# Performance work log

Hardware: AMD Instinct MI355X
Metric: run time of the kernel (lower is better)

The kernel has to match this reference:

```python
import jax, jax.numpy as jnp
import numpy as np

B, S, C, H = 2, 4096, 1024, 16
DH = C // H  # 64
# diffusers: attn.scale = dim_head ** -0.5; code divides scores by scale**0.5
SCALE = 1.0 / (float(DH) ** -0.25)  # == DH ** 0.25


def setup_inputs() -> dict:
    key = jax.random.key(0)
    ks = jax.random.split(key, 6)
    w = 0.02
    return {
        "hidden_states": jax.random.normal(ks[0], (B, S, C), jnp.float32),
        "Wq": jax.random.normal(ks[1], (C, C), jnp.float32) * w,
        "Wk": jax.random.normal(ks[2], (C, C), jnp.float32) * w,
        "Wv": jax.random.normal(ks[3], (C, C), jnp.float32) * w,
        "Wo": jax.random.normal(ks[4], (C, C), jnp.float32) * w,
        "bo": jnp.zeros((C,), jnp.float32),
        # token sizes >= 1 (number of patches each token represents)
        "token_sizes": jax.random.randint(ks[5], (B, S), 1, 17, jnp.int32),
    }


def _split_heads(x):
    # [B, S, C] -> [B, H, S, DH]
    return x.reshape(B, S, H, DH).transpose(0, 2, 1, 3)


def reference(hidden_states, Wq, Wk, Wv, Wo, bo, token_sizes):
    q = _split_heads(hidden_states @ Wq)  # [B,H,S,DH]
    k = _split_heads(hidden_states @ Wk)
    v = _split_heads(hidden_states @ Wv)
    # QK^T with diffusers-style scaling: scores / attn.scale**0.5 == scores * DH**0.25
    scores = jnp.einsum("bhqd,bhkd->bhqk", q, k) * SCALE  # [B,H,S,S]
    # additive log(token_size) bias over keys (self-attention path)
    log_sizes = jnp.log(token_sizes.astype(jnp.float32))  # [B,S]
    scores = scores + log_sizes[:, None, None, :]
    probs = jax.nn.softmax(scores, axis=-1)
    out = jnp.einsum("bhqk,bhkd->bhqd", probs, v)  # [B,H,S,DH]
    out = out.transpose(0, 2, 1, 3).reshape(B, S, C)  # merge heads
    return out @ Wo + bo  # to_out[0] linear; to_out[1] dropout is identity
```

## Files before the change

kernel.cpp:

```cpp
#include <hip/hip_runtime.h>


typedef unsigned short u16;
typedef unsigned int u32;
typedef _Float16 f16x8 __attribute__((ext_vector_type(8)));
typedef float f32x4 __attribute__((ext_vector_type(4)));
typedef short short4v __attribute__((ext_vector_type(4)));

constexpr int SEQ = 4096, CDIM = 1024, NH = 16, DHE = 64;
constexpr float SCALE2 = 2.8284271247461903f * 1.4426950408889634f;

union Frag { f16x8 v; short4v h[2]; };

__device__ __forceinline__ u16 f2h(float f) {
  union { _Float16 h; u16 u; } x;
  x.h = (_Float16)f;
  return x.u;
}

__device__ __forceinline__ u32 pkrtz(float a, float b) {
  u32 r;
  asm("v_cvt_pkrtz_f16_f32 %0, %1, %2" : "=v"(r) : "v"(a), "v"(b));
  return r;
}

__device__ __forceinline__ short4v pk4(const f32x4& v) {
  union { u32 w[2]; short4v s; } u;
  u.w[0] = pkrtz(v[0], v[1]);
  u.w[1] = pkrtz(v[2], v[3]);
  return u.s;
}

__device__ __forceinline__ float exp2fast(float x) {
  float r;
  asm("v_exp_f32 %0, %1" : "=v"(r) : "v"(x));
  return r;
}

__device__ __forceinline__ f32x4 mfma16(const Frag& a, const Frag& b, f32x4 c) {
  return __builtin_amdgcn_mfma_f32_16x16x32_f16(a.v, b.v, c, 0, 0, 0);
}


__global__ void cast_x_kernel(const float* __restrict__ x, u16* __restrict__ out) {
  size_t i = ((size_t)blockIdx.x * 256 + threadIdx.x) * 8;
  float4 a = *(const float4*)(x + i);
  float4 b = *(const float4*)(x + i + 4);
  uint4 o;
  o.x = (u32)f2h(a.x) | ((u32)f2h(a.y) << 16);
  o.y = (u32)f2h(a.z) | ((u32)f2h(a.w) << 16);
  o.z = (u32)f2h(b.x) | ((u32)f2h(b.y) << 16);
  o.w = (u32)f2h(b.z) | ((u32)f2h(b.w) << 16);
  *(uint4*)(out + i) = o;
}

__global__ __launch_bounds__(256) void transpose_w4_kernel(
    const float* __restrict__ Wq, const float* __restrict__ Wk,
    const float* __restrict__ Wv, const float* __restrict__ Wo,
    u16* __restrict__ dq, u16* __restrict__ dk,
    u16* __restrict__ dv, u16* __restrict__ dow) {
  __shared__ float tile[64][65];
  const float* src;
  u16* dst;
  switch (blockIdx.z) {
    case 0: src = Wq; dst = dq; break;
    case 1: src = Wk; dst = dk; break;
    case 2: src = Wv; dst = dv; break;
    default: src = Wo; dst = dow; break;
  }
  const int r0 = blockIdx.y * 64, c0 = blockIdx.x * 64;
  const int tx = threadIdx.x & 63, ty = threadIdx.x >> 6;
#pragma unroll
  for (int i = 0; i < 16; ++i) {
    const int row = i * 4 + ty;
    tile[row][tx] = src[(size_t)(r0 + row) * 1024 + c0 + tx];
  }
  __syncthreads();
#pragma unroll
  for (int i = 0; i < 16; ++i) {
    const int row = i * 4 + ty;
    dst[(size_t)(c0 + row) * 1024 + r0 + tx] = f2h(tile[tx][row]);
  }
}

__global__ void logsz_kernel(const int* __restrict__ ts, float* __restrict__ out) {
  int i = blockIdx.x * 256 + threadIdx.x;
  out[i] = log2f((float)ts[i]);
}


template <int EPI>
__global__ __launch_bounds__(256) void gemm_f16(const u16* __restrict__ A,
                                                const u16* __restrict__ Bt,
                                                void* __restrict__ Out,
                                                const float* __restrict__ bias) {
  __shared__ __align__(16) short Alds[128][40];
  __shared__ __align__(16) short Blds[128][40];
  const int t = threadIdx.x;
  const int bnb = blockIdx.x;
  const int bm = blockIdx.y;
  const int lane = t & 63, wv = t >> 6;
  const int wm = wv >> 1, wn = wv & 1;
  const int l16 = lane & 15, lq = lane >> 4;

  f32x4 acc[4][4];
  f32x4 z = {0.f, 0.f, 0.f, 0.f};
#pragma unroll
  for (int i = 0; i < 4; ++i)
#pragma unroll
    for (int j = 0; j < 4; ++j) acc[i][j] = z;

  const int srow = (t * 8) >> 5;
  const int scol = (t * 8) & 31;

  for (int kb = 0; kb < 32; ++kb) {
    const int k0 = kb * 32;
#pragma unroll
    for (int i = 0; i < 2; ++i) {
      const int row = srow + i * 64;
      uint4 va = *(const uint4*)(A + (size_t)(bm * 128 + row) * 1024 + k0 + scol);
      *(uint4*)&Alds[row][scol] = va;
      uint4 vb = *(const uint4*)(Bt + (size_t)(bnb * 128 + row) * 1024 + k0 + scol);
      *(uint4*)&Blds[row][scol] = vb;
    }
    __syncthreads();

    Frag af[4], bf[4];
#pragma unroll
    for (int am = 0; am < 4; ++am) {
      const short* p = &Alds[wm * 64 + am * 16 + l16][lq * 4];
      af[am].h[0] = *(const short4v*)p;
      af[am].h[1] = *(const short4v*)(p + 16);
    }
#pragma unroll
    for (int bn = 0; bn < 4; ++bn) {
      const short* p = &Blds[wn * 64 + bn * 16 + l16][lq * 4];
      bf[bn].h[0] = *(const short4v*)p;
      bf[bn].h[1] = *(const short4v*)(p + 16);
    }
#pragma unroll
    for (int am = 0; am < 4; ++am)
#pragma unroll
      for (int bn = 0; bn < 4; ++bn) acc[am][bn] = mfma16(af[am], bf[bn], acc[am][bn]);
    __syncthreads();
  }

#pragma unroll
  for (int am = 0; am < 4; ++am) {
#pragma unroll
    for (int bn = 0; bn < 4; ++bn) {
#pragma unroll
      for (int r = 0; r < 4; ++r) {
        const int m = bm * 128 + wm * 64 + am * 16 + lq * 4 + r;
        const int n = bnb * 128 + wn * 64 + bn * 16 + l16;
        const float vsum = acc[am][bn][r];
        if (EPI == 0) {
          const int which = n >> 10;
          const int nn = n & 1023;
          const int h = nn >> 6, d = nn & 63;
          const int b = m >> 12, s = m & 4095;
          const int bhh = b * NH + h;
          size_t addr;
          if (which == 2)
            addr = (size_t)2 * 8388608 + ((size_t)bhh * DHE + d) * SEQ + s;
          else
            addr = (size_t)which * 8388608 + ((size_t)bhh * SEQ + s) * DHE + d;
          ((u16*)Out)[addr] = f2h(vsum);
        } else {
          ((float*)Out)[(size_t)m * 1024 + n] = vsum + bias[n];
        }
      }
    }
  }
}


__global__ __launch_bounds__(256) void attn_kernel(const u16* __restrict__ Q,
                                                   const u16* __restrict__ K,
                                                   const u16* __restrict__ Vt,
                                                   const float* __restrict__ logsz,
                                                   u16* __restrict__ Out) {
  __shared__ __align__(16) short Klds[2][64][72];
  __shared__ __align__(16) short Vtlds[2][64][72];

  const int t = threadIdx.x;
  const int bh = blockIdx.x >> 5;
  const int qb = blockIdx.x & 31;
  const int lane = t & 63, wv = t >> 6;
  const int l16 = lane & 15, lq = lane >> 4;
  const int b = bh >> 4, h = bh & 15;

  Frag qf[2][2];
#pragma unroll
  for (int qh = 0; qh < 2; ++qh) {
    const int qrow = qb * 128 + wv * 32 + qh * 16 + l16;
    const u16* qp = Q + ((size_t)bh * SEQ + qrow) * DHE;
#pragma unroll
    for (int f = 0; f < 2; ++f) {
      qf[qh][f].h[0] = *(const short4v*)(qp + f * 32 + lq * 4);
      qf[qh][f].h[1] = *(const short4v*)(qp + f * 32 + lq * 4 + 16);
    }
  }

  Frag ones;
  {
    short4v o1 = {0x3C00, 0x3C00, 0x3C00, 0x3C00};
    ones.h[0] = o1; ones.h[1] = o1;
  }

  float mrow[2] = {-1e30f, -1e30f};
  f32x4 lsum[2];
  f32x4 oacc[2][4];
  f32x4 z = {0.f, 0.f, 0.f, 0.f};
  lsum[0] = z; lsum[1] = z;
#pragma unroll
  for (int qh = 0; qh < 2; ++qh)
#pragma unroll
    for (int d = 0; d < 4; ++d) oacc[qh][d] = z;

  const int a7 = t & 7, sd = a7 * 8, skey = t >> 3;
  const int vd = t >> 2, voct = (t & 3) * 8;
  const int vsw = ((vd >> 3) & 7) << 3;

  const u16* Kbase = K + (size_t)bh * SEQ * DHE;
  const u16* Vtbase = Vt + ((size_t)bh * DHE + vd) * SEQ;
  const float* lbase = logsz + b * SEQ;

  uint4 kv0 = *(const uint4*)(Kbase + (size_t)skey * DHE + sd);
  uint4 kv1 = *(const uint4*)(Kbase + (size_t)(skey + 32) * DHE + sd);
  uint4 vv0 = *(const uint4*)(Vtbase + voct);
  uint4 vv1 = *(const uint4*)(Vtbase + voct + 32);

  for (int kt = 0; kt < 64; ++kt) {
    short (*Kb)[72] = Klds[kt & 1];
    short (*Vb)[72] = Vtlds[kt & 1];
    *(uint4*)&Kb[skey][sd] = kv0;
    *(uint4*)&Kb[skey + 32][sd] = kv1;
    *(uint4*)&Vb[vd][voct ^ vsw] = vv0;
    *(uint4*)&Vb[vd][(voct + 32) ^ vsw] = vv1;

    if (kt < 63) {
      const u16* Kn = Kbase + (size_t)(kt + 1) * 64 * DHE + (size_t)skey * DHE + sd;
      kv0 = *(const uint4*)(Kn);
      kv1 = *(const uint4*)(Kn + 32 * DHE);
      const u16* Vn = Vtbase + (kt + 1) * 64 + voct;
      vv0 = *(const uint4*)(Vn);
      vv1 = *(const uint4*)(Vn + 32);
    }
    __syncthreads();

    f32x4 lg4[4];
#pragma unroll
    for (int k2 = 0; k2 < 4; ++k2)
      lg4[k2] = *(const f32x4*)(lbase + kt * 64 + k2 * 16 + lq * 4);

    f32x4 sc[2][4];
#pragma unroll
    for (int k2 = 0; k2 < 4; ++k2) {
      Frag kfr[2];
#pragma unroll
      for (int f = 0; f < 2; ++f) {
        const short* p = &Kb[k2 * 16 + l16][f * 32 + lq * 4];
        kfr[f].h[0] = *(const short4v*)p;
        kfr[f].h[1] = *(const short4v*)(p + 16);
      }
#pragma unroll
      for (int qh = 0; qh < 2; ++qh) {
        f32x4 a = mfma16(kfr[0], qf[qh][0], z);
        a = mfma16(kfr[1], qf[qh][1], a);
        sc[qh][k2] = a;
      }
    }

    Frag paf[2][2];
#pragma unroll
    for (int qh = 0; qh < 2; ++qh) {
      float hm[4];
#pragma unroll
      for (int k2 = 0; k2 < 4; ++k2) {
        f32x4 s = sc[qh][k2] * SCALE2 + lg4[k2];
        sc[qh][k2] = s;
        hm[k2] = fmaxf(fmaxf(s[0], s[1]), fmaxf(s[2], s[3]));
      }
      float mx = fmaxf(fmaxf(hm[0], hm[1]), fmaxf(hm[2], hm[3]));
      mx = fmaxf(mx, __shfl_xor(mx, 16));
      mx = fmaxf(mx, __shfl_xor(mx, 32));
      if (__any(mx > mrow[qh] + 8.f)) {
        const float mn = fmaxf(mrow[qh], mx);
        const float alpha = exp2fast(mrow[qh] - mn);
        mrow[qh] = mn;
        f32x4 alv;
#pragma unroll
        for (int r = 0; r < 4; ++r) alv[r] = __shfl(alpha, lq * 4 + r, 16);
#pragma unroll
        for (int dd = 0; dd < 4; ++dd) oacc[qh][dd] *= alv;
        lsum[qh] *= alv;
      }
      const float m2 = mrow[qh];
#pragma unroll
      for (int k2 = 0; k2 < 4; ++k2) {
        f32x4 s = sc[qh][k2];
#pragma unroll
        for (int r = 0; r < 4; ++r) s[r] = exp2fast(s[r] - m2);
        sc[qh][k2] = s;
      }
      paf[qh][0].h[0] = pk4(sc[qh][0]); paf[qh][0].h[1] = pk4(sc[qh][1]);
      paf[qh][1].h[0] = pk4(sc[qh][2]); paf[qh][1].h[1] = pk4(sc[qh][3]);
      lsum[qh] = mfma16(paf[qh][0], ones, lsum[qh]);
      lsum[qh] = mfma16(paf[qh][1], ones, lsum[qh]);
    }

#pragma unroll
    for (int dd = 0; dd < 4; ++dd) {
      const int vrow = dd * 16 + l16;
      const int e = ((vrow >> 3) & 7) << 3;
#pragma unroll
      for (int kh = 0; kh < 2; ++kh) {
        Frag vb;
        vb.h[0] = *(const short4v*)&Vb[vrow][(kh * 32 + lq * 4) ^ e];
        vb.h[1] = *(const short4v*)&Vb[vrow][(kh * 32 + 16 + lq * 4) ^ e];
        oacc[0][dd] = mfma16(paf[0][kh], vb, oacc[0][dd]);
        oacc[1][dd] = mfma16(paf[1][kh], vb, oacc[1][dd]);
      }
    }
  }

#pragma unroll
  for (int qh = 0; qh < 2; ++qh) {
    f32x4 linv;
#pragma unroll
    for (int r = 0; r < 4; ++r) linv[r] = 1.f / lsum[qh][r];
#pragma unroll
    for (int dd = 0; dd < 4; ++dd) {
#pragma unroll
      for (int r = 0; r < 4; ++r) {
        const int row = qb * 128 + wv * 32 + qh * 16 + lq * 4 + r;
        const float v = oacc[qh][dd][r] * linv[r];
        Out[((size_t)b * SEQ + row) * CDIM + h * DHE + dd * 16 + l16] = f2h(v);
      }
    }
  }
}


extern "C" void kernel_launch(void* const* d_in, const int* in_sizes, int n_in,
                              void* d_out, int out_size, void* d_ws, size_t ws_size,
                              hipStream_t stream) {
  const float* hs = (const float*)d_in[0];
  const float* Wq = (const float*)d_in[1];
  const float* Wk = (const float*)d_in[2];
  const float* Wv = (const float*)d_in[3];
  const float* Wo = (const float*)d_in[4];
  const float* bo = (const float*)d_in[5];
  const int* ts = (const int*)d_in[6];
  float* out = (float*)d_out;

  char* ws = (char*)d_ws;
  u16* xf = (u16*)(ws);
  u16* wtq = (u16*)(ws + 16777216);
  u16* wtk = (u16*)(ws + 18874368);
  u16* wtv = (u16*)(ws + 20971520);
  u16* wto = (u16*)(ws + 23068672);
  u16* qbuf = (u16*)(ws + 25165824);
  u16* kbuf = (u16*)(ws + 41943040);
  u16* vtbuf = (u16*)(ws + 58720256);
  float* lsz = (float*)(ws + 75497472);

  cast_x_kernel<<<4096, 256, 0, stream>>>(hs, xf);
  transpose_w4_kernel<<<dim3(16, 16, 4), 256, 0, stream>>>(Wq, Wk, Wv, Wo,
                                                           wtq, wtk, wtv, wto);
  logsz_kernel<<<32, 256, 0, stream>>>(ts, lsz);

  gemm_f16<0><<<dim3(24, 64), 256, 0, stream>>>(xf, wtq, (void*)qbuf, nullptr);

  attn_kernel<<<1024, 256, 0, stream>>>(qbuf, kbuf, vtbuf, lsz, xf);

  gemm_f16<1><<<dim3(8, 64), 256, 0, stream>>>(xf, wto, (void*)out, bo);

  (void)in_sizes; (void)n_in; (void)out_size; (void)ws_size;
}
```

Before: 398.8 us.

## Fold token-size bias into V and row-sum weights, prescale Q, seed MFMA with negative max

The additive log(token_size) bias moves out of the attention loop. V rows are multiplied by token size in the QKV GEMM epilogue, and the row sum is computed by MFMA against the fp16 token sizes instead of a vector of ones. Q is prescaled by the softmax scale in the same epilogue, and the running max is subtracted by seeding the QK MFMA accumulator with -m. Together these remove the per-element scale, bias add and max subtract from the inner loop. In exchange, V scaled by up to 16 in fp16 loses some headroom, and the max is now taken over unbiased scores, which changes the numerical behaviour slightly.

```diff
diff --git a/kernel.cpp b/kernel.cpp
--- a/kernel.cpp
+++ b/kernel.cpp
@@ -83,9 +83,9 @@
   }
 }
 
-__global__ void logsz_kernel(const int* __restrict__ ts, float* __restrict__ out) {
+__global__ void tscast_kernel(const int* __restrict__ ts, u16* __restrict__ out) {
   int i = blockIdx.x * 256 + threadIdx.x;
-  out[i] = log2f((float)ts[i]);
+  out[i] = f2h((float)ts[i]);
 }
 
 
@@ -93,7 +93,8 @@
 __global__ __launch_bounds__(256) void gemm_f16(const u16* __restrict__ A,
                                                 const u16* __restrict__ Bt,
                                                 void* __restrict__ Out,
-                                                const float* __restrict__ bias) {
+                                                const float* __restrict__ bias,
+                                                const int* __restrict__ ts) {
   __shared__ __align__(16) short Alds[128][40];
   __shared__ __align__(16) short Blds[128][40];
   const int t = threadIdx.x;
@@ -153,7 +154,7 @@
       for (int r = 0; r < 4; ++r) {
         const int m = bm * 128 + wm * 64 + am * 16 + lq * 4 + r;
         const int n = bnb * 128 + wn * 64 + bn * 16 + l16;
-        const float vsum = acc[am][bn][r];
+        float vsum = acc[am][bn][r];
         if (EPI == 0) {
           const int which = n >> 10;
           const int nn = n & 1023;
@@ -161,10 +162,13 @@
           const int b = m >> 12, s = m & 4095;
           const int bhh = b * NH + h;
           size_t addr;
-          if (which == 2)
+          if (which == 2) {
+            vsum *= (float)ts[b * SEQ + s];
             addr = (size_t)2 * 8388608 + ((size_t)bhh * DHE + d) * SEQ + s;
-          else
+          } else {
+            if (which == 0) vsum *= SCALE2;
             addr = (size_t)which * 8388608 + ((size_t)bhh * SEQ + s) * DHE + d;
+          }
           ((u16*)Out)[addr] = f2h(vsum);
         } else {
           ((float*)Out)[(size_t)m * 1024 + n] = vsum + bias[n];
@@ -178,7 +182,7 @@
 __global__ __launch_bounds__(256) void attn_kernel(const u16* __restrict__ Q,
                                                    const u16* __restrict__ K,
                                                    const u16* __restrict__ Vt,
-                                                   const float* __restrict__ logsz,
+                                                   const u16* __restrict__ ts16,
                                                    u16* __restrict__ Out) {
   __shared__ __align__(16) short Klds[2][64][72];
   __shared__ __align__(16) short Vtlds[2][64][72];
@@ -202,13 +206,7 @@
     }
   }
 
-  Frag ones;
-  {
-    short4v o1 = {0x3C00, 0x3C00, 0x3C00, 0x3C00};
-    ones.h[0] = o1; ones.h[1] = o1;
-  }
-
-  float mrow[2] = {-1e30f, -1e30f};
+  float mrow[2] = {0.f, 0.f};
   f32x4 lsum[2];
   f32x4 oacc[2][4];
   f32x4 z = {0.f, 0.f, 0.f, 0.f};
@@ -224,7 +222,7 @@
 
   const u16* Kbase = K + (size_t)bh * SEQ * DHE;
   const u16* Vtbase = Vt + ((size_t)bh * DHE + vd) * SEQ;
-  const float* lbase = logsz + b * SEQ;
+  const u16* tsb = ts16 + b * SEQ;
 
   uint4 kv0 = *(const uint4*)(Kbase + (size_t)skey * DHE + sd);
   uint4 kv1 = *(const uint4*)(Kbase + (size_t)(skey + 32) * DHE + sd);
@@ -249,12 +247,23 @@
     }
     __syncthreads();
 
-    f32x4 lg4[4];
-#pragma unroll
-    for (int k2 = 0; k2 < 4; ++k2)
-      lg4[k2] = *(const f32x4*)(lbase + kt * 64 + k2 * 16 + lq * 4);
+    Frag tsfr[2];
+    {
+      const u16* tst = tsb + kt * 64;
+#pragma unroll
+      for (int kh = 0; kh < 2; ++kh) {
+        tsfr[kh].h[0] = *(const short4v*)(tst + kh * 32 + lq * 4);
+        tsfr[kh].h[1] = *(const short4v*)(tst + kh * 32 + lq * 4 + 16);
+      }
+    }
 
     f32x4 sc[2][4];
+    f32x4 seed[2];
+#pragma unroll
+    for (int qh = 0; qh < 2; ++qh) {
+      const float nm = -mrow[qh];
+      seed[qh][0] = nm; seed[qh][1] = nm; seed[qh][2] = nm; seed[qh][3] = nm;
+    }
 #pragma unroll
     for (int k2 = 0; k2 < 4; ++k2) {
       Frag kfr[2];
@@ -266,7 +275,7 @@
       }
 #pragma unroll
       for (int qh = 0; qh < 2; ++qh) {
-        f32x4 a = mfma16(kfr[0], qf[qh][0], z);
+        f32x4 a = mfma16(kfr[0], qf[qh][0], seed[qh]);
         a = mfma16(kfr[1], qf[qh][1], a);
         sc[qh][k2] = a;
       }
@@ -278,36 +287,36 @@
       float hm[4];
 #pragma unroll
       for (int k2 = 0; k2 < 4; ++k2) {
-        f32x4 s = sc[qh][k2] * SCALE2 + lg4[k2];
-        sc[qh][k2] = s;
+        const f32x4 s = sc[qh][k2];
         hm[k2] = fmaxf(fmaxf(s[0], s[1]), fmaxf(s[2], s[3]));
       }
       float mx = fmaxf(fmaxf(hm[0], hm[1]), fmaxf(hm[2], hm[3]));
       mx = fmaxf(mx, __shfl_xor(mx, 16));
       mx = fmaxf(mx, __shfl_xor(mx, 32));
-      if (__any(mx > mrow[qh] + 8.f)) {
-        const float mn = fmaxf(mrow[qh], mx);
-        const float alpha = exp2fast(mrow[qh] - mn);
-        mrow[qh] = mn;
+      if (__any(mx > 8.f)) {
+        const float sh = fmaxf(mx, 0.f);
+        const float al = exp2fast(-sh);
+        mrow[qh] += sh;
         f32x4 alv;
 #pragma unroll
-        for (int r = 0; r < 4; ++r) alv[r] = __shfl(alpha, lq * 4 + r, 16);
+        for (int r = 0; r < 4; ++r) alv[r] = __shfl(al, lq * 4 + r, 16);
 #pragma unroll
         for (int dd = 0; dd < 4; ++dd) oacc[qh][dd] *= alv;
         lsum[qh] *= alv;
-      }
-      const float m2 = mrow[qh];
+#pragma unroll
+        for (int k2 = 0; k2 < 4; ++k2) sc[qh][k2] -= sh;
+      }
 #pragma unroll
       for (int k2 = 0; k2 < 4; ++k2) {
         f32x4 s = sc[qh][k2];
 #pragma unroll
-        for (int r = 0; r < 4; ++r) s[r] = exp2fast(s[r] - m2);
+        for (int r = 0; r < 4; ++r) s[r] = exp2fast(s[r]);
         sc[qh][k2] = s;
       }
       paf[qh][0].h[0] = pk4(sc[qh][0]); paf[qh][0].h[1] = pk4(sc[qh][1]);
       paf[qh][1].h[0] = pk4(sc[qh][2]); paf[qh][1].h[1] = pk4(sc[qh][3]);
-      lsum[qh] = mfma16(paf[qh][0], ones, lsum[qh]);
-      lsum[qh] = mfma16(paf[qh][1], ones, lsum[qh]);
+      lsum[qh] = mfma16(paf[qh][0], tsfr[0], lsum[qh]);
+      lsum[qh] = mfma16(paf[qh][1], tsfr[1], lsum[qh]);
     }
 
 #pragma unroll
@@ -364,18 +373,18 @@
   u16* qbuf = (u16*)(ws + 25165824);
   u16* kbuf = (u16*)(ws + 41943040);
   u16* vtbuf = (u16*)(ws + 58720256);
-  float* lsz = (float*)(ws + 75497472);
+  u16* ts16 = (u16*)(ws + 75497472);
 
   cast_x_kernel<<<4096, 256, 0, stream>>>(hs, xf);
   transpose_w4_kernel<<<dim3(16, 16, 4), 256, 0, stream>>>(Wq, Wk, Wv, Wo,
                                                            wtq, wtk, wtv, wto);
-  logsz_kernel<<<32, 256, 0, stream>>>(ts, lsz);
-
-  gemm_f16<0><<<dim3(24, 64), 256, 0, stream>>>(xf, wtq, (void*)qbuf, nullptr);
-
-  attn_kernel<<<1024, 256, 0, stream>>>(qbuf, kbuf, vtbuf, lsz, xf);
-
-  gemm_f16<1><<<dim3(8, 64), 256, 0, stream>>>(xf, wto, (void*)out, bo);
+  tscast_kernel<<<32, 256, 0, stream>>>(ts, ts16);
+
+  gemm_f16<0><<<dim3(24, 64), 256, 0, stream>>>(xf, wtq, (void*)qbuf, nullptr, ts);
+
+  attn_kernel<<<1024, 256, 0, stream>>>(qbuf, kbuf, vtbuf, ts16, xf);
+
+  gemm_f16<1><<<dim3(8, 64), 256, 0, stream>>>(xf, wto, (void*)out, bo, nullptr);
 
   (void)in_sizes; (void)n_in; (void)out_size; (void)ws_size;
 }
```

Measured after the change: 402.3 us. No clear change (+0.9%).
